# Optimization experiments

Hardware: AMD Instinct MI355X
Metric: run time of the kernel (lower is better)

Reference implementation:

```python
import jax, jax.numpy as jnp
import numpy as np

UNITS = 1024
NCLASS = 8000
BATCH = 4096

def setup_inputs() -> dict:
    key = jax.random.key(0)
    k1, k2, k3, k4 = jax.random.split(key, 4)
    inputs = jax.random.randint(k1, (BATCH, 1), 0, NCLASS, dtype=jnp.int32)
    h_tm1 = jax.random.normal(k2, (BATCH, UNITS), dtype=jnp.float32)
    # orthogonal-ish recurrent kernel (scaled normal is fine for a numeric reference)
    recurrent_kernel = jax.random.normal(k3, (UNITS, 4 * UNITS), dtype=jnp.float32) * (1.0 / np.sqrt(UNITS))
    kernel_c = jax.random.normal(k4, (NCLASS, 4 * UNITS), dtype=jnp.float32) * (1.0 / np.sqrt(NCLASS))
    bias_z = jnp.full((UNITS,), 5.0, dtype=jnp.float32)  # initializer=constant(5)
    bias = jnp.zeros((3 * UNITS,), dtype=jnp.float32)
    return {"inputs": inputs, "h_tm1": h_tm1, "recurrent_kernel": recurrent_kernel,
            "kernel_c": kernel_c, "bias_z": bias_z, "bias": bias}

def reference(inputs, h_tm1, recurrent_kernel, kernel_c, bias_z, bias):
    u = h_tm1.shape[-1]
    ch = inputs[:, 0].astype(jnp.int32)
    # one_hot(ch) @ kernel_c == row gather of kernel_c (identical math, O(1) per row)
    c_proj = kernel_c[ch]                      # [B, 4u]
    cz, cr, ch_, co = (c_proj[:, :u], c_proj[:, u:2*u], c_proj[:, 2*u:3*u], c_proj[:, 3*u:])
    Rz, Rr, Rh, Ro = (recurrent_kernel[:, :u], recurrent_kernel[:, u:2*u],
                      recurrent_kernel[:, 2*u:3*u], recurrent_kernel[:, 3*u:])
    z = jax.nn.sigmoid(h_tm1 @ Rz + cz + bias_z)
    r = jax.nn.sigmoid(h_tm1 @ Rr + cr + bias[:u])
    hh = jnp.tanh((r * h_tm1) @ Rh + ch_ + bias[u:2*u])
    h = z * h_tm1 + (1.0 - z) * hh
    o = jnp.tanh(h @ Ro + co + bias[2*u:])
    return (o, h)
```

## Files before the change

kernel.cpp:

```cpp
#include <hip/hip_runtime.h>
#include <stdint.h>

#define UNITS 1024
#define BATCH 4096
#define FOURU 4096

typedef __bf16 bf16x8 __attribute__((ext_vector_type(8)));
typedef float f32x4 __attribute__((ext_vector_type(4)));

__device__ __forceinline__ uint16_t f2bf(float f) {
  uint32_t u = __builtin_bit_cast(uint32_t, f);
  u += 0x7FFFu + ((u >> 16) & 1u);
  return (uint16_t)(u >> 16);
}

__device__ __forceinline__ float fsig(float x) {
  return 1.0f / (1.0f + __expf(-x));
}

__device__ __forceinline__ f32x4 mfma16x16x32(bf16x8 a, bf16x8 b, f32x4 c) {
  return __builtin_amdgcn_mfma_f32_16x16x32_bf16(a, b, c, 0, 0, 0);
}

template <int NG>
__device__ __forceinline__ void stage_tile(const uint16_t* __restrict__ src,
                                           uint4* lds, int tid) {
#pragma unroll
  for (int p = 0; p < NG / 256; ++p) {
    int gi = p * 256 + tid;
    lds[gi] = *(const uint4*)(src + (gi >> 2) * UNITS + (gi & 3) * 8);
  }
}

__global__ __launch_bounds__(256) void convert_kernel(const float* __restrict__ in,
                                                      uint16_t* __restrict__ out) {
  const int i = (blockIdx.x * 256 + threadIdx.x) * 4;
  float4 v = *(const float4*)(in + i);
  ushort4 o;
  o.x = f2bf(v.x); o.y = f2bf(v.y); o.z = f2bf(v.z); o.w = f2bf(v.w);
  *(ushort4*)(out + i) = o;
}

__global__ __launch_bounds__(256) void transpose_kernel(const float* __restrict__ R,
                                                        uint16_t* __restrict__ RT) {
  __shared__ float t[32][33];
  const int n0 = blockIdx.x * 32, k0 = blockIdx.y * 32;
  const int tx = threadIdx.x & 31, ty = threadIdx.x >> 5;
#pragma unroll
  for (int i = 0; i < 4; ++i)
    t[ty + i * 8][tx] = R[(k0 + ty + i * 8) * FOURU + n0 + tx];
  __syncthreads();
#pragma unroll
  for (int i = 0; i < 4; ++i)
    RT[(n0 + ty + i * 8) * UNITS + k0 + tx] = f2bf(t[tx][ty + i * 8]);
}

__global__ __launch_bounds__(256) void s1_kernel(
    const uint16_t* __restrict__ hbf, const uint16_t* __restrict__ rt,
    const int* __restrict__ idx, const float* __restrict__ kc,
    const float* __restrict__ bz, const float* __restrict__ bias,
    const float* __restrict__ h32, float* __restrict__ zbuf,
    uint16_t* __restrict__ rhb) {
  __shared__ uint4 sA[512], sBz[256], sBr[256];
  const int tid = threadIdx.x;
  const int lane = tid & 63, wave = tid >> 6;
  const int l15 = lane & 15, l4 = lane >> 4;
  const int row0 = blockIdx.y * 128, col0 = blockIdx.x * 64;
  const int rb = (wave >> 1) * 64, cb = (wave & 1) * 32;

  const uint16_t* pa = hbf + row0 * UNITS;
  const uint16_t* pbz = rt + col0 * UNITS;
  const uint16_t* pbr = rt + (UNITS + col0) * UNITS;

  f32x4 accZ[4][2] = {};
  f32x4 accR[4][2] = {};

  for (int k0 = 0; k0 < UNITS; k0 += 32) {
    stage_tile<512>(pa + k0, sA, tid);
    stage_tile<256>(pbz + k0, sBz, tid);
    stage_tile<256>(pbr + k0, sBr, tid);
    __syncthreads();
    const bf16x8* A8 = (const bf16x8*)sA;
    const bf16x8* Bz8 = (const bf16x8*)sBz;
    const bf16x8* Br8 = (const bf16x8*)sBr;
    bf16x8 af[4], bzf[2], brf[2];
#pragma unroll
    for (int m = 0; m < 4; ++m) af[m] = A8[(rb + m * 16 + l15) * 4 + l4];
#pragma unroll
    for (int n = 0; n < 2; ++n) {
      bzf[n] = Bz8[(cb + n * 16 + l15) * 4 + l4];
      brf[n] = Br8[(cb + n * 16 + l15) * 4 + l4];
    }
#pragma unroll
    for (int m = 0; m < 4; ++m)
#pragma unroll
      for (int n = 0; n < 2; ++n) {
        accZ[m][n] = mfma16x16x32(af[m], bzf[n], accZ[m][n]);
        accR[m][n] = mfma16x16x32(af[m], brf[n], accR[m][n]);
      }
    __syncthreads();
  }

#pragma unroll
  for (int m = 0; m < 4; ++m) {
#pragma unroll
    for (int q = 0; q < 4; ++q) {
      const int i = row0 + rb + m * 16 + l4 * 4 + q;
      const int ch = idx[i];
      const float* kcrow = kc + ch * FOURU;
#pragma unroll
      for (int n = 0; n < 2; ++n) {
        const int j = col0 + cb + n * 16 + l15;
        const int ij = i * UNITS + j;
        float z = fsig(accZ[m][n][q] + kcrow[j] + bz[j]);
        float r = fsig(accR[m][n][q] + kcrow[UNITS + j] + bias[j]);
        float hv = h32[ij];
        zbuf[ij] = z;
        rhb[ij] = f2bf(r * hv);
      }
    }
  }
}

template <int MODE>
__global__ __launch_bounds__(256) void s23_kernel(
    const uint16_t* __restrict__ abf, const uint16_t* __restrict__ bt,
    const int* __restrict__ idx, const float* __restrict__ kc,
    const float* __restrict__ bias, const float* __restrict__ h32,
    const float* __restrict__ zbuf, float* __restrict__ out32,
    uint16_t* __restrict__ outbf) {
  __shared__ uint4 sA[512], sB[256];
  const int tid = threadIdx.x;
  const int lane = tid & 63, wave = tid >> 6;
  const int l15 = lane & 15, l4 = lane >> 4;
  const int row0 = blockIdx.y * 128, col0 = blockIdx.x * 64;
  const int rb = (wave >> 1) * 64, cb = (wave & 1) * 32;
  const uint16_t* pa = abf + row0 * UNITS;
  const uint16_t* pb = bt + col0 * UNITS;
  f32x4 acc[4][2] = {};

  for (int k0 = 0; k0 < UNITS; k0 += 32) {
    stage_tile<512>(pa + k0, sA, tid);
    stage_tile<256>(pb + k0, sB, tid);
    __syncthreads();
    const bf16x8* A8 = (const bf16x8*)sA;
    const bf16x8* B8 = (const bf16x8*)sB;
    bf16x8 af[4], bff[2];
#pragma unroll
    for (int m = 0; m < 4; ++m) af[m] = A8[(rb + m * 16 + l15) * 4 + l4];
#pragma unroll
    for (int n = 0; n < 2; ++n) bff[n] = B8[(cb + n * 16 + l15) * 4 + l4];
#pragma unroll
    for (int m = 0; m < 4; ++m)
#pragma unroll
      for (int n = 0; n < 2; ++n)
        acc[m][n] = mfma16x16x32(af[m], bff[n], acc[m][n]);
    __syncthreads();
  }

#pragma unroll
  for (int m = 0; m < 4; ++m) {
#pragma unroll
    for (int q = 0; q < 4; ++q) {
      const int i = row0 + rb + m * 16 + l4 * 4 + q;
      const int ch = idx[i];
      const float* kcrow = kc + ch * FOURU;
#pragma unroll
      for (int n = 0; n < 2; ++n) {
        const int j = col0 + cb + n * 16 + l15;
        const int ij = i * UNITS + j;
        if (MODE == 0) {
          float hh = tanhf(acc[m][n][q] + kcrow[2 * UNITS + j] + bias[UNITS + j]);
          float z = zbuf[ij];
          float hv = h32[ij];
          float hn = z * hv + (1.0f - z) * hh;
          out32[ij] = hn;
          outbf[ij] = f2bf(hn);
        } else {
          float o = tanhf(acc[m][n][q] + kcrow[3 * UNITS + j] + bias[2 * UNITS + j]);
          out32[ij] = o;
        }
      }
    }
  }
}

extern "C" void kernel_launch(void* const* d_in, const int* in_sizes, int n_in,
                              void* d_out, int out_size, void* d_ws, size_t ws_size,
                              hipStream_t stream) {
  const int* idx = (const int*)d_in[0];
  const float* h32 = (const float*)d_in[1];
  const float* R = (const float*)d_in[2];
  const float* kc = (const float*)d_in[3];
  const float* bz = (const float*)d_in[4];
  const float* bias = (const float*)d_in[5];

  float* o_out = (float*)d_out;
  float* h_out = o_out + (size_t)BATCH * UNITS;

  uint16_t* hbf = (uint16_t*)d_ws;
  uint16_t* rt = hbf + (size_t)BATCH * UNITS;
  uint16_t* rhb = rt + (size_t)FOURU * UNITS;
  uint16_t* hnb = rhb + (size_t)BATCH * UNITS;
  float* zbuf = o_out;

  convert_kernel<<<dim3(BATCH * UNITS / 1024), 256, 0, stream>>>(h32, hbf);
  transpose_kernel<<<dim3(FOURU / 32, UNITS / 32), 256, 0, stream>>>(R, rt);
  s1_kernel<<<dim3(UNITS / 64, BATCH / 128), 256, 0, stream>>>(
      hbf, rt, idx, kc, bz, bias, h32, zbuf, rhb);
  s23_kernel<0><<<dim3(UNITS / 64, BATCH / 128), 256, 0, stream>>>(
      rhb, rt + (size_t)2 * UNITS * UNITS, idx, kc, bias, h32, zbuf, h_out, hnb);
  s23_kernel<1><<<dim3(UNITS / 64, BATCH / 128), 256, 0, stream>>>(
      hnb, rt + (size_t)3 * UNITS * UNITS, idx, kc, bias, nullptr, nullptr, o_out, nullptr);
}
```

Baseline: 129.0 us.

## Double-buffer GEMM tiles via direct global-to-LDS loads and store z in bf16

Stages A and B tiles with global_load_lds straight into LDS and double-buffers them, prefetching the next K-slice while the current one is consumed by MFMA, with one barrier per iteration instead of two. The gate buffer z is stored as bf16 in workspace instead of fp32 in the output, and s1 reads h from the bf16 copy rather than the fp32 input. This cuts epilogue memory traffic and hides load latency, at the cost of doubled LDS use and extra bf16 rounding of z and r*h. Prefetching into the other buffer without waiting on the async LDS writes before the next barrier depends on correct vmcnt handling.

```diff
diff --git a/kernel.cpp b/kernel.cpp
--- a/kernel.cpp
+++ b/kernel.cpp
@@ -13,22 +13,31 @@
   u += 0x7FFFu + ((u >> 16) & 1u);
   return (uint16_t)(u >> 16);
 }
-
+__device__ __forceinline__ float bf2f(uint16_t b) {
+  uint32_t u = ((uint32_t)b) << 16;
+  return __builtin_bit_cast(float, u);
+}
 __device__ __forceinline__ float fsig(float x) {
   return 1.0f / (1.0f + __expf(-x));
 }
-
 __device__ __forceinline__ f32x4 mfma16x16x32(bf16x8 a, bf16x8 b, f32x4 c) {
   return __builtin_amdgcn_mfma_f32_16x16x32_bf16(a, b, c, 0, 0, 0);
 }
 
+__device__ __forceinline__ void gll16(uint16_t* lds, const uint16_t* g) {
+  __builtin_amdgcn_global_load_lds(
+      (const __attribute__((address_space(1))) uint32_t*)g,
+      (__attribute__((address_space(3))) uint32_t*)lds, 16, 0, 0);
+}
+
 template <int NG>
-__device__ __forceinline__ void stage_tile(const uint16_t* __restrict__ src,
-                                           uint4* lds, int tid) {
+__device__ __forceinline__ void stage(const uint16_t* __restrict__ src,
+                                      uint16_t* lds, int tid) {
+  const int wb = tid & 192;
 #pragma unroll
   for (int p = 0; p < NG / 256; ++p) {
-    int gi = p * 256 + tid;
-    lds[gi] = *(const uint4*)(src + (gi >> 2) * UNITS + (gi & 3) * 8);
+    const int gi = p * 256 + tid;
+    gll16(lds + (p * 256 + wb) * 8, src + (gi >> 2) * UNITS + (gi & 3) * 8);
   }
 }
 
@@ -59,9 +68,10 @@
     const uint16_t* __restrict__ hbf, const uint16_t* __restrict__ rt,
     const int* __restrict__ idx, const float* __restrict__ kc,
     const float* __restrict__ bz, const float* __restrict__ bias,
-    const float* __restrict__ h32, float* __restrict__ zbuf,
-    uint16_t* __restrict__ rhb) {
-  __shared__ uint4 sA[512], sBz[256], sBr[256];
+    uint16_t* __restrict__ zb, uint16_t* __restrict__ rhb) {
+  __shared__ uint16_t sA[2][512 * 8];
+  __shared__ uint16_t sBz[2][256 * 8];
+  __shared__ uint16_t sBr[2][256 * 8];
   const int tid = threadIdx.x;
   const int lane = tid & 63, wave = tid >> 6;
   const int l15 = lane & 15, l4 = lane >> 4;
@@ -75,14 +85,21 @@
   f32x4 accZ[4][2] = {};
   f32x4 accR[4][2] = {};
 
+  stage<512>(pa, sA[0], tid);
+  stage<256>(pbz, sBz[0], tid);
+  stage<256>(pbr, sBr[0], tid);
+  __syncthreads();
+
+  int cur = 0;
   for (int k0 = 0; k0 < UNITS; k0 += 32) {
-    stage_tile<512>(pa + k0, sA, tid);
-    stage_tile<256>(pbz + k0, sBz, tid);
-    stage_tile<256>(pbr + k0, sBr, tid);
-    __syncthreads();
-    const bf16x8* A8 = (const bf16x8*)sA;
-    const bf16x8* Bz8 = (const bf16x8*)sBz;
-    const bf16x8* Br8 = (const bf16x8*)sBr;
+    if (k0 + 32 < UNITS) {
+      stage<512>(pa + k0 + 32, sA[cur ^ 1], tid);
+      stage<256>(pbz + k0 + 32, sBz[cur ^ 1], tid);
+      stage<256>(pbr + k0 + 32, sBr[cur ^ 1], tid);
+    }
+    const bf16x8* A8 = (const bf16x8*)sA[cur];
+    const bf16x8* Bz8 = (const bf16x8*)sBz[cur];
+    const bf16x8* Br8 = (const bf16x8*)sBr[cur];
     bf16x8 af[4], bzf[2], brf[2];
 #pragma unroll
     for (int m = 0; m < 4; ++m) af[m] = A8[(rb + m * 16 + l15) * 4 + l4];
@@ -99,6 +116,7 @@
         accR[m][n] = mfma16x16x32(af[m], brf[n], accR[m][n]);
       }
     __syncthreads();
+    cur ^= 1;
   }
 
 #pragma unroll
@@ -114,8 +132,8 @@
         const int ij = i * UNITS + j;
         float z = fsig(accZ[m][n][q] + kcrow[j] + bz[j]);
         float r = fsig(accR[m][n][q] + kcrow[UNITS + j] + bias[j]);
-        float hv = h32[ij];
-        zbuf[ij] = z;
+        float hv = bf2f(hbf[ij]);
+        zb[ij] = f2bf(z);
         rhb[ij] = f2bf(r * hv);
       }
     }
@@ -127,9 +145,10 @@
     const uint16_t* __restrict__ abf, const uint16_t* __restrict__ bt,
     const int* __restrict__ idx, const float* __restrict__ kc,
     const float* __restrict__ bias, const float* __restrict__ h32,
-    const float* __restrict__ zbuf, float* __restrict__ out32,
+    const uint16_t* __restrict__ zb, float* __restrict__ out32,
     uint16_t* __restrict__ outbf) {
-  __shared__ uint4 sA[512], sB[256];
+  __shared__ uint16_t sA[2][512 * 8];
+  __shared__ uint16_t sB[2][256 * 8];
   const int tid = threadIdx.x;
   const int lane = tid & 63, wave = tid >> 6;
   const int l15 = lane & 15, l4 = lane >> 4;
@@ -139,12 +158,18 @@
   const uint16_t* pb = bt + col0 * UNITS;
   f32x4 acc[4][2] = {};
 
+  stage<512>(pa, sA[0], tid);
+  stage<256>(pb, sB[0], tid);
+  __syncthreads();
+
+  int cur = 0;
   for (int k0 = 0; k0 < UNITS; k0 += 32) {
-    stage_tile<512>(pa + k0, sA, tid);
-    stage_tile<256>(pb + k0, sB, tid);
-    __syncthreads();
-    const bf16x8* A8 = (const bf16x8*)sA;
-    const bf16x8* B8 = (const bf16x8*)sB;
+    if (k0 + 32 < UNITS) {
+      stage<512>(pa + k0 + 32, sA[cur ^ 1], tid);
+      stage<256>(pb + k0 + 32, sB[cur ^ 1], tid);
+    }
+    const bf16x8* A8 = (const bf16x8*)sA[cur];
+    const bf16x8* B8 = (const bf16x8*)sB[cur];
     bf16x8 af[4], bff[2];
 #pragma unroll
     for (int m = 0; m < 4; ++m) af[m] = A8[(rb + m * 16 + l15) * 4 + l4];
@@ -156,6 +181,7 @@
       for (int n = 0; n < 2; ++n)
         acc[m][n] = mfma16x16x32(af[m], bff[n], acc[m][n]);
     __syncthreads();
+    cur ^= 1;
   }
 
 #pragma unroll
@@ -171,7 +197,7 @@
         const int ij = i * UNITS + j;
         if (MODE == 0) {
           float hh = tanhf(acc[m][n][q] + kcrow[2 * UNITS + j] + bias[UNITS + j]);
-          float z = zbuf[ij];
+          float z = bf2f(zb[ij]);
           float hv = h32[ij];
           float hn = z * hv + (1.0f - z) * hh;
           out32[ij] = hn;
@@ -202,12 +228,12 @@
   uint16_t* rt = hbf + (size_t)BATCH * UNITS;
   uint16_t* rhb = rt + (size_t)FOURU * UNITS;
   uint16_t* hnb = rhb + (size_t)BATCH * UNITS;
-  float* zbuf = o_out;
+  uint16_t* zbuf = hnb + (size_t)BATCH * UNITS;
 
   convert_kernel<<<dim3(BATCH * UNITS / 1024), 256, 0, stream>>>(h32, hbf);
   transpose_kernel<<<dim3(FOURU / 32, UNITS / 32), 256, 0, stream>>>(R, rt);
   s1_kernel<<<dim3(UNITS / 64, BATCH / 128), 256, 0, stream>>>(
-      hbf, rt, idx, kc, bz, bias, h32, zbuf, rhb);
+      hbf, rt, idx, kc, bz, bias, zbuf, rhb);
   s23_kernel<0><<<dim3(UNITS / 64, BATCH / 128), 256, 0, stream>>>(
       rhb, rt + (size_t)2 * UNITS * UNITS, idx, kc, bias, h32, zbuf, h_out, hnb);
   s23_kernel<1><<<dim3(UNITS / 64, BATCH / 128), 256, 0, stream>>>(
```

After: 121.3 us. 5.9% less time.
